# Kernel optimization log

Hardware: AMD Instinct MI355X
Metric: run time of the kernel (lower is better)

Reference implementation:

```python
import jax, jax.numpy as jnp
import numpy as np

PHI = 1.6
JITTER = 1e-4
ETA = 1.0
BETA = 0.5
EPS_CHOL = 1e-6
R_NEIGH = 2


def _solve3(L, d):
    # lower-triangular 3x3 forward substitution; L broadcasts against d[..., 3]
    y0 = d[..., 0] / L[..., 0, 0]
    y1 = (d[..., 1] - L[..., 1, 0] * y0) / L[..., 1, 1]
    y2 = (d[..., 2] - L[..., 2, 0] * y0 - L[..., 2, 1] * y1) / L[..., 2, 2]
    return jnp.stack([y0, y1, y2], axis=-1)


def _overlap_score(delta, L):
    # fused_gaussian_overlap_score: Gaussian log-overlap ~ -0.5*(Mahalanobis + logdet)
    y = _solve3(L, delta)
    maha = jnp.sum(y * y, axis=-1)
    logdet = 2.0 * jnp.sum(jnp.log(jnp.diagonal(L, axis1=-2, axis2=-1)), axis=-1)
    return -0.5 * (maha + logdet)


def _head(x, ln_g, ln_b, W1, b1, W2, b2):
    # LayerNorm -> Linear -> SiLU -> Linear(->1), squeeze
    m = jnp.mean(x, axis=-1, keepdims=True)
    v = jnp.var(x, axis=-1, keepdims=True)
    h = (x - m) / jnp.sqrt(v + 1e-5) * ln_g + ln_b
    h = jax.nn.silu(h @ W1 + b1)
    return (h @ W2 + b2)[..., 0]


def setup_inputs() -> dict:
    key = jax.random.key(0)
    ks = jax.random.split(key, 12)
    B, Kp, M, C = 2, 1024, 8, 256
    s_parent = jax.random.normal(ks[0], (B, Kp, C), jnp.float32)
    mu_p = jax.random.normal(ks[1], (B, Kp, 3), jnp.float32) * 10.0
    A = jax.random.normal(ks[2], (B, Kp, 3, 3), jnp.float32) * 0.5
    Sigma_p = jnp.einsum('bkij,bklj->bkil', A, A) + 0.05 * jnp.eye(3, dtype=jnp.float32)
    mask_parent = jnp.ones((B, Kp), jnp.float32)
    xi_noise = jax.random.normal(ks[3], (B, Kp, M, 3), jnp.float32)
    emb = jax.random.normal(ks[4], (M, C), jnp.float32) * 0.02
    lin = lambda k, fi, fo, s=0.02: jax.random.normal(k, (fi, fo), jnp.float32) * s
    return dict(
        s_parent=s_parent, mu_p=mu_p, Sigma_p=Sigma_p, mask_parent=mask_parent,
        xi_noise=xi_noise, emb=emb,
        gate_ln_g=jnp.ones((C,), jnp.float32), gate_ln_b=jnp.zeros((C,), jnp.float32),
        gate_W1=lin(ks[5], C, C), gate_b1=jnp.zeros((C,), jnp.float32),
        gate_W2=lin(ks[6], C, 1), gate_b2=jnp.zeros((1,), jnp.float32),
        prior_ln_g=jnp.ones((C,), jnp.float32), prior_ln_b=jnp.zeros((C,), jnp.float32),
        prior_W1=lin(ks[7], C, C), prior_b1=jnp.zeros((C,), jnp.float32),
        prior_W2=lin(ks[8], C, 1), prior_b2=jnp.zeros((1,), jnp.float32),
        geom_W=lin(ks[9], C, 3, 0.01), geom_b=jnp.zeros((3,), jnp.float32),
        K_target=6144,
    )


def reference(s_parent, mu_p, Sigma_p, mask_parent, xi_noise, emb,
              gate_ln_g, gate_ln_b, gate_W1, gate_b1, gate_W2, gate_b2,
              prior_ln_g, prior_ln_b, prior_W1, prior_b1, prior_W2, prior_b2,
              geom_W, geom_b, K_target):
    B, Kp, C = s_parent.shape
    M = emb.shape[0]
    Kc = Kp * M
    I3 = jnp.eye(3, dtype=s_parent.dtype)

    # --- candidate children from per-parent Cholesky splat ---
    Lp = jnp.linalg.cholesky(Sigma_p + EPS_CHOL * I3)               # [B,Kp,3,3]
    xi = xi_noise + (emb @ geom_W + geom_b)                          # [B,Kp,M,3]
    mu0 = mu_p[:, :, None, :] + jnp.einsum('bkae,bkme->bkma', Lp, xi)
    mu0 = mu0.reshape(B, Kc, 3)

    j0 = jnp.repeat(jnp.arange(Kp), M)                               # [Kc] birth parent
    t_ids = jnp.tile(jnp.arange(M), Kp)                              # [Kc] child slot
    m0 = mask_parent[:, j0]

    # --- gate g ---
    gate_in = s_parent[:, j0, :] + emb[t_ids]                        # [B,Kc,C]
    b = _head(gate_in, gate_ln_g, gate_ln_b, gate_W1, gate_b1, gate_W2, gate_b2)
    a = jax.nn.softplus(_head(s_parent, prior_ln_g, prior_ln_b, prior_W1, prior_b1, prior_W2, prior_b2))
    b = b + BETA * jnp.log(a[:, j0] + 1e-8)
    g = jax.nn.sigmoid(b / max(ETA, 1e-6)) * m0                      # [B,Kc]
    loss_count = jnp.mean((jnp.sum(g, axis=1) - float(K_target)) ** 2)

    # --- top-R neighbor parents by overlap score (indices only, no grad) ---
    mu0_birth = mu_p[:, j0, :]                                       # mu of birth parent
    delta1 = mu0_birth[:, :, None, :] - mu_p[:, None, :, :]          # [B,Kc,Kp,3]
    score1 = _overlap_score(delta1, Lp[:, None])                     # [B,Kc,Kp]
    self_hot = (jnp.arange(Kp)[None, :] == j0[:, None])              # [Kc,Kp]
    score1 = jnp.where(self_hot[None], 1e9, score1)
    _, neigh = jax.lax.top_k(jax.lax.stop_gradient(score1), R_NEIGH) # [B,Kc,R], col0=j0

    bidx = jnp.arange(B)[:, None, None]
    mu_nei = mu_p[bidx, neigh]                                       # [B,Kc,R,3]
    Sig_nei = Sigma_p[bidx, neigh]                                   # [B,Kc,R,3,3]
    L_nei = Lp[bidx, neigh]
    s_nei = s_parent[bidx, neigh]                                    # [B,Kc,R,C]

    # --- soft responsibilities over the R neighbors ---
    score2 = _overlap_score(mu0[:, :, None, :] - mu_nei, L_nei)      # [B,Kc,R]
    w = jax.nn.softmax(score2, axis=-1)

    # --- moment-matching refine (sparse form of B_resp: rows of B are w scattered at neigh) ---
    mu_child = jnp.einsum('bir,bird->bid', w, mu_nei)                # [B,Kc,3]
    intra = jnp.einsum('bir,birmn->bimn', w, Sig_nei) * PHI ** (-2)
    dmu = mu_nei - mu_child[:, :, None, :]
    inter = jnp.einsum('bir,birm,birn->bimn', w, dmu, dmu)
    Sigma_child = intra + inter + JITTER * I3                        # [B,Kc,3,3]

    s_mix = jnp.einsum('bir,birc->bic', w, s_nei)
    s_child0 = g[..., None] * s_mix                                  # [B,Kc,C]
    return s_child0, mu_child, Sigma_child, g, loss_count
```

## Files before the change

### kernel.cpp

```cpp
#include <hip/hip_runtime.h>
#include <math.h>

#define NPAR 2048
#define KP   1024
#define MM   8
#define CC   256
#define KC   8192
#define NCH  16384

#define WS_PKL    0
#define WS_PKI    8192
#define WS_PKM    16384
#define WS_L22    24576
#define WS_MEANSP 26624
#define WS_SUMSQ  28672
#define WS_DOT8   30720
#define WS_APRIOR 47104
#define WS_EGATE  49152
#define WS_UGATE  51200
#define WS_C0GATE 51456
#define WS_GEO    51712
#define WS_MEANE  51736
#define WS_SUMSQE 51744
#define WS_NEIGH  51752
#define WS_PGATE  53824

#define OUT_S    0
#define OUT_MU   4194304
#define OUT_SIG  4243456
#define OUT_G    4390912
#define OUT_LOSS 4407296

__device__ __forceinline__ float siluf(float x){ return x / (1.f + expf(-x)); }
__device__ __forceinline__ float softplusf(float x){ return x > 20.f ? x : log1pf(expf(x)); }

__global__ __launch_bounds__(256) void kP1(const float* __restrict__ sp,
                                           const float* __restrict__ mu_p,
                                           const float* __restrict__ Sig,
                                           const float* __restrict__ emb,
                                           const float* __restrict__ geom_W,
                                           const float* __restrict__ geom_b,
                                           float* __restrict__ ws) {
  int blk = blockIdx.x;
  int t = threadIdx.x;
  if (blk < 512) {
    int pid  = blk * 4 + (t >> 6);
    int lane = t & 63;
    const float4 v = *(const float4*)(sp + pid * CC + lane * 4);
    float s  = v.x + v.y + v.z + v.w;
    float ss = v.x*v.x + v.y*v.y + v.z*v.z + v.w*v.w;
    float pd[8];
#pragma unroll
    for (int m = 0; m < 8; m++) {
      float4 e = *(const float4*)(emb + m * CC + lane * 4);
      pd[m] = v.x*e.x + v.y*e.y + v.z*e.z + v.w*e.w;
    }
#pragma unroll
    for (int o = 32; o > 0; o >>= 1) {
      s  += __shfl_xor(s, o);
      ss += __shfl_xor(ss, o);
#pragma unroll
      for (int m = 0; m < 8; m++) pd[m] += __shfl_xor(pd[m], o);
    }
    if (lane == 0) {
      ws[WS_MEANSP + pid] = s * (1.f / 256.f);
      ws[WS_SUMSQ + pid]  = ss;
#pragma unroll
      for (int m = 0; m < 8; m++) ws[WS_DOT8 + pid * 8 + m] = pd[m];
    }
  } else if (blk < 520) {
    int pid = (blk - 512) * 256 + t;
    const float* S = Sig + pid * 9;
    float a00 = S[0] + 1e-6f, a10 = S[3], a11 = S[4] + 1e-6f;
    float a20 = S[6], a21 = S[7], a22 = S[8] + 1e-6f;
    float L00 = sqrtf(a00); float i0 = 1.f / L00;
    float L10 = a10 * i0, L20 = a20 * i0;
    float L11 = sqrtf(a11 - L10 * L10); float i1 = 1.f / L11;
    float L21 = (a21 - L20 * L10) * i1;
    float L22 = sqrtf(a22 - L20 * L20 - L21 * L21); float i2 = 1.f / L22;
    float logdet = 2.f * logf(L00 * L11 * L22);
    float4 pkl = {L10, L20, L21, logdet};
    float4 pki = {i0, i1, i2, L00};
    float4 pkm = {mu_p[pid*3+0], mu_p[pid*3+1], mu_p[pid*3+2], L11};
    *(float4*)(ws + WS_PKL + pid * 4) = pkl;
    *(float4*)(ws + WS_PKI + pid * 4) = pki;
    *(float4*)(ws + WS_PKM + pid * 4) = pkm;
    ws[WS_L22 + pid] = L22;
  } else {
    if (t < 192) {
      int o = t >> 3, lane8 = t & 7;
      int m = o / 3, d = o % 3;
      float acc = 0.f;
      for (int k = lane8; k < 256; k += 8) acc += emb[m * 256 + k] * geom_W[k * 3 + d];
      acc += __shfl_xor(acc, 1); acc += __shfl_xor(acc, 2); acc += __shfl_xor(acc, 4);
      if (lane8 == 0) ws[WS_GEO + o] = acc + geom_b[d];
    } else {
      int o = (t - 192) >> 3, lane8 = t & 7;
      if (o < 8) {
        float s = 0.f, ss = 0.f;
        for (int k = lane8; k < 256; k += 8) { float e = emb[o * 256 + k]; s += e; ss += e * e; }
        s  += __shfl_xor(s, 1);  s  += __shfl_xor(s, 2);  s  += __shfl_xor(s, 4);
        ss += __shfl_xor(ss, 1); ss += __shfl_xor(ss, 2); ss += __shfl_xor(ss, 4);
        if (lane8 == 0) { ws[WS_MEANE + o] = s * (1.f / 256.f); ws[WS_SUMSQE + o] = ss; }
      }
    }
  }
}

__global__ __launch_bounds__(256) void kP2(const float* __restrict__ sp,
                                           const float* __restrict__ emb,
                                           const float* __restrict__ g_ln_g,
                                           const float* __restrict__ g_ln_b,
                                           const float* __restrict__ gW1,
                                           const float* __restrict__ gb1,
                                           const float* __restrict__ p_ln_g,
                                           const float* __restrict__ p_ln_b,
                                           const float* __restrict__ pW1,
                                           const float* __restrict__ pb1,
                                           const float* __restrict__ pW2,
                                           const float* __restrict__ pb2,
                                           float* __restrict__ ws) {
  __shared__ float xs[8][256];
  __shared__ float red[4][8];
  __shared__ float redS[4][8];
  __shared__ float redQ[4][8];
  __shared__ float mv[2][8];
  int blk = blockIdx.x;
  int t = threadIdx.x;

  if (blk < 512) {
    int wv = blk * 4 + (t >> 6);
    int lane = t & 63;
    int b = wv >> 10;
    int j = wv & (KP - 1);
    const float4 qm = *(const float4*)(ws + WS_PKM + wv * 4);
    float qx = qm.x, qy = qm.y, qz = qm.z;
    float best = -3.4e38f; int bidx = 1 << 30;
    for (int it = 0; it < 16; it++) {
      int k = it * 64 + lane;
      int idx = b * KP + k;
      float4 pl = *(const float4*)(ws + WS_PKL + idx * 4);
      float4 pi = *(const float4*)(ws + WS_PKI + idx * 4);
      float4 pm = *(const float4*)(ws + WS_PKM + idx * 4);
      float dx = qx - pm.x, dy = qy - pm.y, dz = qz - pm.z;
      float y0 = dx * pi.x;
      float y1 = (dy - pl.x * y0) * pi.y;
      float y2 = (dz - pl.y * y0 - pl.z * y1) * pi.z;
      float sc = -0.5f * (y0*y0 + y1*y1 + y2*y2 + pl.w);
      if (k == j) sc = -3.4e38f;
      if (sc > best || (sc == best && k < bidx)) { best = sc; bidx = k; }
    }
#pragma unroll
    for (int o = 32; o > 0; o >>= 1) {
      float ob = __shfl_xor(best, o);
      int   oi = __shfl_xor(bidx, o);
      if (ob > best || (ob == best && oi < bidx)) { best = ob; bidx = oi; }
    }
    if (lane == 0) ((int*)ws)[WS_NEIGH + wv] = bidx;
  } else {
    int cblk = blk - 512;
    bool prior = (cblk >= 256 && cblk < 512);
    const float* W1 = prior ? pW1 : gW1;

    if (cblk < 256) {
      int base = cblk * 8;
      float g = g_ln_g[t];
#pragma unroll
      for (int r = 0; r < 8; r++) xs[r][t] = sp[(base + r) * 256 + t] * g;
    } else if (cblk < 512) {
      int base = (cblk - 256) * 8;
      float vr[8], s1[8], s2[8];
#pragma unroll
      for (int r = 0; r < 8; r++) {
        vr[r] = sp[(base + r) * 256 + t];
        s1[r] = vr[r];
        s2[r] = vr[r] * vr[r];
      }
#pragma unroll
      for (int o = 32; o > 0; o >>= 1) {
#pragma unroll
        for (int r = 0; r < 8; r++) { s1[r] += __shfl_xor(s1[r], o); s2[r] += __shfl_xor(s2[r], o); }
      }
      int wave = t >> 6;
      if ((t & 63) == 0) {
#pragma unroll
        for (int r = 0; r < 8; r++) { redS[wave][r] = s1[r]; redQ[wave][r] = s2[r]; }
      }
      __syncthreads();
      if (t < 8) {
        float sum = redS[0][t] + redS[1][t] + redS[2][t] + redS[3][t];
        float sq  = redQ[0][t] + redQ[1][t] + redQ[2][t] + redQ[3][t];
        float mean = sum * (1.f / 256.f);
        float var  = sq * (1.f / 256.f) - mean * mean;
        mv[0][t] = mean;
        mv[1][t] = rsqrtf(var + 1e-5f);
      }
      __syncthreads();
      float pg = p_ln_g[t], pbv = p_ln_b[t];
#pragma unroll
      for (int r = 0; r < 8; r++)
        xs[r][t] = (vr[r] - mv[0][r]) * mv[1][r] * pg + pbv;
    } else if (cblk == 512) {
      float g = g_ln_g[t];
#pragma unroll
      for (int r = 0; r < 8; r++) xs[r][t] = emb[r * 256 + t] * g;
    } else {
      xs[0][t] = g_ln_g[t];
      xs[1][t] = g_ln_b[t];
#pragma unroll
      for (int r = 2; r < 8; r++) xs[r][t] = 0.f;
    }
    __syncthreads();

    float acc[8] = {0,0,0,0,0,0,0,0};
    for (int k4 = 0; k4 < 256; k4 += 4) {
      float w0 = W1[(k4+0) * 256 + t];
      float w1 = W1[(k4+1) * 256 + t];
      float w2 = W1[(k4+2) * 256 + t];
      float w3 = W1[(k4+3) * 256 + t];
#pragma unroll
      for (int r = 0; r < 8; r++) {
        float4 x4 = *(const float4*)&xs[r][k4];
        acc[r] += x4.x * w0 + x4.y * w1 + x4.z * w2 + x4.w * w3;
      }
    }

    if (cblk < 256) {
      int base = cblk * 8;
#pragma unroll
      for (int r = 0; r < 8; r++) ws[WS_PGATE + (base + r) * 256 + t] = acc[r];
    } else if (cblk < 512) {
      int base = (cblk - 256) * 8;
      float b1 = pb1[t], w2 = pW2[t];
      float tv[8];
#pragma unroll
      for (int r = 0; r < 8; r++) {
        float h = acc[r] + b1;
        tv[r] = siluf(h) * w2;
      }
#pragma unroll
      for (int o = 32; o > 0; o >>= 1) {
#pragma unroll
        for (int r = 0; r < 8; r++) tv[r] += __shfl_xor(tv[r], o);
      }
      int wave = t >> 6;
      if ((t & 63) == 0) {
#pragma unroll
        for (int r = 0; r < 8; r++) red[wave][r] = tv[r];
      }
      __syncthreads();
      if (t < 8) {
        float sum = red[0][t] + red[1][t] + red[2][t] + red[3][t] + pb2[0];
        ws[WS_APRIOR + base + t] = softplusf(sum);
      }
    } else if (cblk == 512) {
#pragma unroll
      for (int r = 0; r < 8; r++) ws[WS_EGATE + r * 256 + t] = acc[r];
    } else {
      ws[WS_UGATE + t]  = acc[0];
      ws[WS_C0GATE + t] = acc[1] + gb1[t];
    }
  }
}

__global__ __launch_bounds__(256) void kD(const float* __restrict__ sp,
                                          const float* __restrict__ Sig,
                                          const float* __restrict__ mask,
                                          const float* __restrict__ xi_noise,
                                          const float* __restrict__ gW2,
                                          const float* __restrict__ gb2,
                                          const float* __restrict__ ws,
                                          float* __restrict__ out) {
  int wv   = blockIdx.x * 4 + (threadIdx.x >> 6);
  int lane = threadIdx.x & 63;
  int b = wv >> 13;
  int i = wv & (KC - 1);
  int j = i >> 3;
  int m = i & 7;
  int prow = b * KP + j;

  float mean_x = ws[WS_MEANSP + prow] + ws[WS_MEANE + m];
  float Ex2 = ws[WS_SUMSQ + prow] + 2.f * ws[WS_DOT8 + prow * 8 + m] + ws[WS_SUMSQE + m];
  float var = Ex2 * (1.f / 256.f) - mean_x * mean_x;
  float rstd = rsqrtf(var + 1e-5f);

  int c4 = lane * 4;
  float Pv[4], Ev[4], Uv[4], C0v[4], W2v[4];
  *(float4*)Pv  = *(const float4*)(ws + WS_PGATE + prow * 256 + c4);
  *(float4*)Ev  = *(const float4*)(ws + WS_EGATE + m * 256 + c4);
  *(float4*)Uv  = *(const float4*)(ws + WS_UGATE + c4);
  *(float4*)C0v = *(const float4*)(ws + WS_C0GATE + c4);
  *(float4*)W2v = *(const float4*)(gW2 + c4);
  float partial = 0.f;
#pragma unroll
  for (int q = 0; q < 4; q++) {
    float pre = (Pv[q] + Ev[q] - mean_x * Uv[q]) * rstd + C0v[q];
    partial += siluf(pre) * W2v[q];
  }
#pragma unroll
  for (int o = 32; o > 0; o >>= 1) partial += __shfl_xor(partial, o);
  float aP = ws[WS_APRIOR + prow];
  float bval = partial + gb2[0] + 0.5f * logf(aP + 1e-8f);
  float g = (1.f / (1.f + expf(-bval))) * mask[prow];

  const float4 plP = *(const float4*)(ws + WS_PKL + prow * 4);
  const float4 piP = *(const float4*)(ws + WS_PKI + prow * 4);
  const float4 pmP = *(const float4*)(ws + WS_PKM + prow * 4);
  float L22 = ws[WS_L22 + prow];

  int xbase = (prow * 8 + m) * 3;
  float x0 = xi_noise[xbase + 0] + ws[WS_GEO + m * 3 + 0];
  float x1 = xi_noise[xbase + 1] + ws[WS_GEO + m * 3 + 1];
  float x2 = xi_noise[xbase + 2] + ws[WS_GEO + m * 3 + 2];
  float m0x = pmP.x + piP.w * x0;
  float m0y = pmP.y + plP.x * x0 + pmP.w * x1;
  float m0z = pmP.z + plP.y * x0 + plP.z * x1 + L22 * x2;

  int n1 = ((const int*)ws)[WS_NEIGH + prow];
  int nrow1 = b * KP + n1;
  const float4 plN = *(const float4*)(ws + WS_PKL + nrow1 * 4);
  const float4 piN = *(const float4*)(ws + WS_PKI + nrow1 * 4);
  const float4 pmN = *(const float4*)(ws + WS_PKM + nrow1 * 4);

  float sc[2], nx[2], ny[2], nz[2];
  {
    float dx = m0x - pmP.x, dy = m0y - pmP.y, dz = m0z - pmP.z;
    float y0 = dx * piP.x;
    float y1 = (dy - plP.x * y0) * piP.y;
    float y2 = (dz - plP.y * y0 - plP.z * y1) * piP.z;
    sc[0] = -0.5f * (y0*y0 + y1*y1 + y2*y2 + plP.w);
    nx[0] = pmP.x; ny[0] = pmP.y; nz[0] = pmP.z;
  }
  {
    float dx = m0x - pmN.x, dy = m0y - pmN.y, dz = m0z - pmN.z;
    float y0 = dx * piN.x;
    float y1 = (dy - plN.x * y0) * piN.y;
    float y2 = (dz - plN.y * y0 - plN.z * y1) * piN.z;
    sc[1] = -0.5f * (y0*y0 + y1*y1 + y2*y2 + plN.w);
    nx[1] = pmN.x; ny[1] = pmN.y; nz[1] = pmN.z;
  }
  float mxs = fmaxf(sc[0], sc[1]);
  float e0 = expf(sc[0] - mxs), e1 = expf(sc[1] - mxs);
  float inv = 1.f / (e0 + e1);
  float w0 = e0 * inv, w1 = e1 * inv;

  float mcx = w0 * nx[0] + w1 * nx[1];
  float mcy = w0 * ny[0] + w1 * ny[1];
  float mcz = w0 * nz[0] + w1 * nz[1];

  float d0x = nx[0] - mcx, d0y = ny[0] - mcy, d0z = nz[0] - mcz;
  float d1x = nx[1] - mcx, d1y = ny[1] - mcy, d1z = nz[1] - mcz;
  const float* S0 = Sig + prow * 9;
  const float* S1 = Sig + nrow1 * 9;
  const float PHIm2 = 0.390625f;
  float Sout[9];
  float dd0[3] = {d0x, d0y, d0z};
  float dd1[3] = {d1x, d1y, d1z};
#pragma unroll
  for (int a = 0; a < 3; a++)
#pragma unroll
    for (int e = 0; e < 3; e++) {
      float v = (w0 * S0[a*3+e] + w1 * S1[a*3+e]) * PHIm2
              + w0 * dd0[a] * dd0[e] + w1 * dd1[a] * dd1[e];
      if (a == e) v += 1e-4f;
      Sout[a*3+e] = v;
    }

  if (lane == 0) {
    float* om = out + OUT_MU + wv * 3;
    om[0] = mcx; om[1] = mcy; om[2] = mcz;
    out[OUT_G + wv] = g;
    float* os = out + OUT_SIG + wv * 9;
#pragma unroll
    for (int q = 0; q < 9; q++) os[q] = Sout[q];
  }

  float s0v[4], s1v[4], ov[4];
  *(float4*)s0v = *(const float4*)(sp + prow * 256 + c4);
  *(float4*)s1v = *(const float4*)(sp + nrow1 * 256 + c4);
  float gw0 = g * w0, gw1 = g * w1;
#pragma unroll
  for (int q = 0; q < 4; q++) ov[q] = gw0 * s0v[q] + gw1 * s1v[q];
  *(float4*)(out + OUT_S + wv * 256 + c4) = *(float4*)ov;
}

__global__ __launch_bounds__(256) void kF(const float* __restrict__ out_in,
                                          const int* __restrict__ Kt,
                                          float* __restrict__ out) {
  __shared__ float red[4][2];
  int t = threadIdx.x;
  const float* gp = out_in + OUT_G;
  float s0 = 0.f, s1 = 0.f;
  for (int it = 0; it < 32; it++) {
    s0 += gp[it * 256 + t];
    s1 += gp[KC + it * 256 + t];
  }
#pragma unroll
  for (int o = 32; o > 0; o >>= 1) {
    s0 += __shfl_xor(s0, o);
    s1 += __shfl_xor(s1, o);
  }
  int wave = t >> 6;
  if ((t & 63) == 0) { red[wave][0] = s0; red[wave][1] = s1; }
  __syncthreads();
  if (t == 0) {
    float S0 = red[0][0] + red[1][0] + red[2][0] + red[3][0];
    float S1 = red[0][1] + red[1][1] + red[2][1] + red[3][1];
    float K = (float)Kt[0];
    float l0 = S0 - K, l1 = S1 - K;
    out[OUT_LOSS] = 0.5f * (l0 * l0 + l1 * l1);
  }
}

extern "C" void kernel_launch(void* const* d_in, const int* in_sizes, int n_in,
                              void* d_out, int out_size, void* d_ws, size_t ws_size,
                              hipStream_t stream) {
  const float* s_parent   = (const float*)d_in[0];
  const float* mu_p       = (const float*)d_in[1];
  const float* Sigma_p    = (const float*)d_in[2];
  const float* mask_par   = (const float*)d_in[3];
  const float* xi_noise   = (const float*)d_in[4];
  const float* emb        = (const float*)d_in[5];
  const float* gate_ln_g  = (const float*)d_in[6];
  const float* gate_ln_b  = (const float*)d_in[7];
  const float* gate_W1    = (const float*)d_in[8];
  const float* gate_b1    = (const float*)d_in[9];
  const float* gate_W2    = (const float*)d_in[10];
  const float* gate_b2    = (const float*)d_in[11];
  const float* prior_ln_g = (const float*)d_in[12];
  const float* prior_ln_b = (const float*)d_in[13];
  const float* prior_W1   = (const float*)d_in[14];
  const float* prior_b1   = (const float*)d_in[15];
  const float* prior_W2   = (const float*)d_in[16];
  const float* prior_b2   = (const float*)d_in[17];
  const float* geom_W     = (const float*)d_in[18];
  const float* geom_b     = (const float*)d_in[19];
  const int*   K_target   = (const int*)d_in[20];

  float* ws  = (float*)d_ws;
  float* out = (float*)d_out;

  kP1<<<521, 256, 0, stream>>>(s_parent, mu_p, Sigma_p, emb, geom_W, geom_b, ws);
  kP2<<<1026, 256, 0, stream>>>(s_parent, emb, gate_ln_g, gate_ln_b, gate_W1, gate_b1,
                                prior_ln_g, prior_ln_b, prior_W1, prior_b1,
                                prior_W2, prior_b2, ws);
  kD<<<NCH / 4, 256, 0, stream>>>(s_parent, Sigma_p, mask_par, xi_noise,
                                  gate_W2, gate_b2, ws, out);
  kF<<<1, 256, 0, stream>>>(out, K_target, out);
}
```

Baseline: 151.7 us.

## Merge preprocessing kernels, recompute Cholesky per block into LDS, pre-reduce gate sums

Folds the two preprocessing kernels into one launch. Each neighbor-search block recomputes the Cholesky factors and means for its whole batch into shared memory instead of reading them from a prior kernel. The per-parent stats (mean, sum of squares, embedding dot products) move into the gate-head blocks, and the geometry/embedding stats get their own extra block. kD now writes per-block gate partial sums so the final reduction reads 4096 values instead of 16384. This removes one launch and its dependency, at the cost of redundant Cholesky work per block and 40KB of LDS, which may lower occupancy.

```diff
diff --git a/kernel.cpp b/kernel.cpp
--- a/kernel.cpp
+++ b/kernel.cpp
@@ -24,6 +24,7 @@
 #define WS_SUMSQE 51744
 #define WS_NEIGH  51752
 #define WS_PGATE  53824
+#define WS_GPART  578112
 
 #define OUT_S    0
 #define OUT_MU   4194304
@@ -34,119 +35,79 @@
 __device__ __forceinline__ float siluf(float x){ return x / (1.f + expf(-x)); }
 __device__ __forceinline__ float softplusf(float x){ return x > 20.f ? x : log1pf(expf(x)); }
 
-__global__ __launch_bounds__(256) void kP1(const float* __restrict__ sp,
-                                           const float* __restrict__ mu_p,
-                                           const float* __restrict__ Sig,
-                                           const float* __restrict__ emb,
-                                           const float* __restrict__ geom_W,
-                                           const float* __restrict__ geom_b,
-                                           float* __restrict__ ws) {
+__global__ __launch_bounds__(256) void kA(const float* __restrict__ sp,
+                                          const float* __restrict__ mu_p,
+                                          const float* __restrict__ Sig,
+                                          const float* __restrict__ emb,
+                                          const float* __restrict__ geom_W,
+                                          const float* __restrict__ geom_b,
+                                          const float* __restrict__ g_ln_g,
+                                          const float* __restrict__ g_ln_b,
+                                          const float* __restrict__ gW1,
+                                          const float* __restrict__ gb1,
+                                          const float* __restrict__ p_ln_g,
+                                          const float* __restrict__ p_ln_b,
+                                          const float* __restrict__ pW1,
+                                          const float* __restrict__ pb1,
+                                          const float* __restrict__ pW2,
+                                          const float* __restrict__ pb2,
+                                          float* __restrict__ ws) {
+  __shared__ float smem[10 * 1024];
   int blk = blockIdx.x;
   int t = threadIdx.x;
+
   if (blk < 512) {
-    int pid  = blk * 4 + (t >> 6);
-    int lane = t & 63;
-    const float4 v = *(const float4*)(sp + pid * CC + lane * 4);
-    float s  = v.x + v.y + v.z + v.w;
-    float ss = v.x*v.x + v.y*v.y + v.z*v.z + v.w*v.w;
-    float pd[8];
-#pragma unroll
-    for (int m = 0; m < 8; m++) {
-      float4 e = *(const float4*)(emb + m * CC + lane * 4);
-      pd[m] = v.x*e.x + v.y*e.y + v.z*e.z + v.w*e.w;
-    }
-#pragma unroll
-    for (int o = 32; o > 0; o >>= 1) {
-      s  += __shfl_xor(s, o);
-      ss += __shfl_xor(ss, o);
-#pragma unroll
-      for (int m = 0; m < 8; m++) pd[m] += __shfl_xor(pd[m], o);
-    }
-    if (lane == 0) {
-      ws[WS_MEANSP + pid] = s * (1.f / 256.f);
-      ws[WS_SUMSQ + pid]  = ss;
-#pragma unroll
-      for (int m = 0; m < 8; m++) ws[WS_DOT8 + pid * 8 + m] = pd[m];
-    }
-  } else if (blk < 520) {
-    int pid = (blk - 512) * 256 + t;
-    const float* S = Sig + pid * 9;
-    float a00 = S[0] + 1e-6f, a10 = S[3], a11 = S[4] + 1e-6f;
-    float a20 = S[6], a21 = S[7], a22 = S[8] + 1e-6f;
-    float L00 = sqrtf(a00); float i0 = 1.f / L00;
-    float L10 = a10 * i0, L20 = a20 * i0;
-    float L11 = sqrtf(a11 - L10 * L10); float i1 = 1.f / L11;
-    float L21 = (a21 - L20 * L10) * i1;
-    float L22 = sqrtf(a22 - L20 * L20 - L21 * L21); float i2 = 1.f / L22;
-    float logdet = 2.f * logf(L00 * L11 * L22);
-    float4 pkl = {L10, L20, L21, logdet};
-    float4 pki = {i0, i1, i2, L00};
-    float4 pkm = {mu_p[pid*3+0], mu_p[pid*3+1], mu_p[pid*3+2], L11};
-    *(float4*)(ws + WS_PKL + pid * 4) = pkl;
-    *(float4*)(ws + WS_PKI + pid * 4) = pki;
-    *(float4*)(ws + WS_PKM + pid * 4) = pkm;
-    ws[WS_L22 + pid] = L22;
-  } else {
-    if (t < 192) {
-      int o = t >> 3, lane8 = t & 7;
-      int m = o / 3, d = o % 3;
-      float acc = 0.f;
-      for (int k = lane8; k < 256; k += 8) acc += emb[m * 256 + k] * geom_W[k * 3 + d];
-      acc += __shfl_xor(acc, 1); acc += __shfl_xor(acc, 2); acc += __shfl_xor(acc, 4);
-      if (lane8 == 0) ws[WS_GEO + o] = acc + geom_b[d];
-    } else {
-      int o = (t - 192) >> 3, lane8 = t & 7;
-      if (o < 8) {
-        float s = 0.f, ss = 0.f;
-        for (int k = lane8; k < 256; k += 8) { float e = emb[o * 256 + k]; s += e; ss += e * e; }
-        s  += __shfl_xor(s, 1);  s  += __shfl_xor(s, 2);  s  += __shfl_xor(s, 4);
-        ss += __shfl_xor(ss, 1); ss += __shfl_xor(ss, 2); ss += __shfl_xor(ss, 4);
-        if (lane8 == 0) { ws[WS_MEANE + o] = s * (1.f / 256.f); ws[WS_SUMSQE + o] = ss; }
-      }
-    }
-  }
-}
-
-__global__ __launch_bounds__(256) void kP2(const float* __restrict__ sp,
-                                           const float* __restrict__ emb,
-                                           const float* __restrict__ g_ln_g,
-                                           const float* __restrict__ g_ln_b,
-                                           const float* __restrict__ gW1,
-                                           const float* __restrict__ gb1,
-                                           const float* __restrict__ p_ln_g,
-                                           const float* __restrict__ p_ln_b,
-                                           const float* __restrict__ pW1,
-                                           const float* __restrict__ pb1,
-                                           const float* __restrict__ pW2,
-                                           const float* __restrict__ pb2,
-                                           float* __restrict__ ws) {
-  __shared__ float xs[8][256];
-  __shared__ float red[4][8];
-  __shared__ float redS[4][8];
-  __shared__ float redQ[4][8];
-  __shared__ float mv[2][8];
-  int blk = blockIdx.x;
-  int t = threadIdx.x;
-
-  if (blk < 512) {
+    int b = blk >> 8;
+#pragma unroll
+    for (int q = 0; q < 4; q++) {
+      int loc = q * 256 + t;
+      int pid = b * KP + loc;
+      const float* S = Sig + pid * 9;
+      float a00 = S[0] + 1e-6f, a10 = S[3], a11 = S[4] + 1e-6f;
+      float a20 = S[6], a21 = S[7], a22 = S[8] + 1e-6f;
+      float L00 = sqrtf(a00); float i0 = 1.f / L00;
+      float L10 = a10 * i0, L20 = a20 * i0;
+      float L11 = sqrtf(a11 - L10 * L10); float i1 = 1.f / L11;
+      float L21 = (a21 - L20 * L10) * i1;
+      float L22 = sqrtf(a22 - L20 * L20 - L21 * L21); float i2 = 1.f / L22;
+      float logdet = 2.f * logf(L00 * L11 * L22);
+      float mx = mu_p[pid * 3 + 0], my = mu_p[pid * 3 + 1], mz = mu_p[pid * 3 + 2];
+      smem[0 * 1024 + loc] = L10;
+      smem[1 * 1024 + loc] = L20;
+      smem[2 * 1024 + loc] = L21;
+      smem[3 * 1024 + loc] = logdet;
+      smem[4 * 1024 + loc] = i0;
+      smem[5 * 1024 + loc] = i1;
+      smem[6 * 1024 + loc] = i2;
+      smem[7 * 1024 + loc] = mx;
+      smem[8 * 1024 + loc] = my;
+      smem[9 * 1024 + loc] = mz;
+      if ((loc >> 2) == (blk & 255)) {
+        float4 pkl = {L10, L20, L21, logdet};
+        float4 pki = {i0, i1, i2, L00};
+        float4 pkm = {mx, my, mz, L11};
+        *(float4*)(ws + WS_PKL + pid * 4) = pkl;
+        *(float4*)(ws + WS_PKI + pid * 4) = pki;
+        *(float4*)(ws + WS_PKM + pid * 4) = pkm;
+        ws[WS_L22 + pid] = L22;
+      }
+    }
+    __syncthreads();
+
     int wv = blk * 4 + (t >> 6);
     int lane = t & 63;
-    int b = wv >> 10;
     int j = wv & (KP - 1);
-    const float4 qm = *(const float4*)(ws + WS_PKM + wv * 4);
-    float qx = qm.x, qy = qm.y, qz = qm.z;
+    float qx = smem[7 * 1024 + j], qy = smem[8 * 1024 + j], qz = smem[9 * 1024 + j];
     float best = -3.4e38f; int bidx = 1 << 30;
     for (int it = 0; it < 16; it++) {
       int k = it * 64 + lane;
-      int idx = b * KP + k;
-      float4 pl = *(const float4*)(ws + WS_PKL + idx * 4);
-      float4 pi = *(const float4*)(ws + WS_PKI + idx * 4);
-      float4 pm = *(const float4*)(ws + WS_PKM + idx * 4);
-      float dx = qx - pm.x, dy = qy - pm.y, dz = qz - pm.z;
-      float y0 = dx * pi.x;
-      float y1 = (dy - pl.x * y0) * pi.y;
-      float y2 = (dz - pl.y * y0 - pl.z * y1) * pi.z;
-      float sc = -0.5f * (y0*y0 + y1*y1 + y2*y2 + pl.w);
+      float dx = qx - smem[7 * 1024 + k];
+      float dy = qy - smem[8 * 1024 + k];
+      float dz = qz - smem[9 * 1024 + k];
+      float y0 = dx * smem[4 * 1024 + k];
+      float y1 = (dy - smem[0 * 1024 + k] * y0) * smem[5 * 1024 + k];
+      float y2 = (dz - smem[1 * 1024 + k] * y0 - smem[2 * 1024 + k] * y1) * smem[6 * 1024 + k];
+      float sc = -0.5f * (y0 * y0 + y1 * y1 + y2 * y2 + smem[3 * 1024 + k]);
       if (k == j) sc = -3.4e38f;
       if (sc > best || (sc == best && k < bidx)) { best = sc; bidx = k; }
     }
@@ -158,6 +119,13 @@
     }
     if (lane == 0) ((int*)ws)[WS_NEIGH + wv] = bidx;
   } else {
+    float (*xs)[256] = (float(*)[256])smem;
+    float* statred   = smem + 2048;
+    float (*redS)[8] = (float(*)[8])(smem + 2432);
+    float (*redQ)[8] = (float(*)[8])(smem + 2464);
+    float (*mv)[8]   = (float(*)[8])(smem + 2496);
+    float (*red)[8]  = (float(*)[8])(smem + 2528);
+
     int cblk = blk - 512;
     bool prior = (cblk >= 256 && cblk < 512);
     const float* W1 = prior ? pW1 : gW1;
@@ -165,8 +133,50 @@
     if (cblk < 256) {
       int base = cblk * 8;
       float g = g_ln_g[t];
-#pragma unroll
-      for (int r = 0; r < 8; r++) xs[r][t] = sp[(base + r) * 256 + t] * g;
+      float vr[8], em[8];
+#pragma unroll
+      for (int r = 0; r < 8; r++) vr[r] = sp[(base + r) * 256 + t];
+#pragma unroll
+      for (int m = 0; m < 8; m++) em[m] = emb[m * 256 + t];
+#pragma unroll
+      for (int r = 0; r < 8; r++) xs[r][t] = vr[r] * g;
+      int wave = t >> 6, lane = t & 63;
+#pragma unroll
+      for (int r = 0; r < 8; r++) {
+        float p0 = vr[r], p1 = vr[r] * vr[r];
+        float d[8];
+#pragma unroll
+        for (int m = 0; m < 8; m++) d[m] = vr[r] * em[m];
+#pragma unroll
+        for (int o = 32; o > 0; o >>= 1) {
+          p0 += __shfl_xor(p0, o);
+          p1 += __shfl_xor(p1, o);
+#pragma unroll
+          for (int m = 0; m < 8; m++) d[m] += __shfl_xor(d[m], o);
+        }
+        if (lane == 0) {
+          float* dst = statred + (wave * 8 + r) * 10;
+          dst[0] = p0; dst[1] = p1;
+#pragma unroll
+          for (int m = 0; m < 8; m++) dst[2 + m] = d[m];
+        }
+      }
+      __syncthreads();
+      if (t < 8) {
+        int r = t;
+        float s = 0.f, ss = 0.f, dd[8] = {0, 0, 0, 0, 0, 0, 0, 0};
+#pragma unroll
+        for (int w = 0; w < 4; w++) {
+          float* srcp = statred + (w * 8 + r) * 10;
+          s += srcp[0]; ss += srcp[1];
+#pragma unroll
+          for (int m = 0; m < 8; m++) dd[m] += srcp[2 + m];
+        }
+        ws[WS_MEANSP + base + r] = s * (1.f / 256.f);
+        ws[WS_SUMSQ + base + r]  = ss;
+#pragma unroll
+        for (int m = 0; m < 8; m++) ws[WS_DOT8 + (base + r) * 8 + m] = dd[m];
+      }
     } else if (cblk < 512) {
       int base = (cblk - 256) * 8;
       float vr[8], s1[8], s2[8];
@@ -204,20 +214,39 @@
       float g = g_ln_g[t];
 #pragma unroll
       for (int r = 0; r < 8; r++) xs[r][t] = emb[r * 256 + t] * g;
-    } else {
+    } else if (cblk == 513) {
       xs[0][t] = g_ln_g[t];
       xs[1][t] = g_ln_b[t];
 #pragma unroll
       for (int r = 2; r < 8; r++) xs[r][t] = 0.f;
+    } else {
+      if (t < 192) {
+        int o = t >> 3, lane8 = t & 7;
+        int m = o / 3, d = o % 3;
+        float acc = 0.f;
+        for (int k = lane8; k < 256; k += 8) acc += emb[m * 256 + k] * geom_W[k * 3 + d];
+        acc += __shfl_xor(acc, 1); acc += __shfl_xor(acc, 2); acc += __shfl_xor(acc, 4);
+        if (lane8 == 0) ws[WS_GEO + o] = acc + geom_b[d];
+      } else {
+        int o = (t - 192) >> 3, lane8 = t & 7;
+        if (o < 8) {
+          float s = 0.f, ss = 0.f;
+          for (int k = lane8; k < 256; k += 8) { float e = emb[o * 256 + k]; s += e; ss += e * e; }
+          s  += __shfl_xor(s, 1);  s  += __shfl_xor(s, 2);  s  += __shfl_xor(s, 4);
+          ss += __shfl_xor(ss, 1); ss += __shfl_xor(ss, 2); ss += __shfl_xor(ss, 4);
+          if (lane8 == 0) { ws[WS_MEANE + o] = s * (1.f / 256.f); ws[WS_SUMSQE + o] = ss; }
+        }
+      }
+      return;
     }
     __syncthreads();
 
-    float acc[8] = {0,0,0,0,0,0,0,0};
+    float acc[8] = {0, 0, 0, 0, 0, 0, 0, 0};
     for (int k4 = 0; k4 < 256; k4 += 4) {
-      float w0 = W1[(k4+0) * 256 + t];
-      float w1 = W1[(k4+1) * 256 + t];
-      float w2 = W1[(k4+2) * 256 + t];
-      float w3 = W1[(k4+3) * 256 + t];
+      float w0 = W1[(k4 + 0) * 256 + t];
+      float w1 = W1[(k4 + 1) * 256 + t];
+      float w2 = W1[(k4 + 2) * 256 + t];
+      float w3 = W1[(k4 + 3) * 256 + t];
 #pragma unroll
       for (int r = 0; r < 8; r++) {
         float4 x4 = *(const float4*)&xs[r][k4];
@@ -269,8 +298,9 @@
                                           const float* __restrict__ xi_noise,
                                           const float* __restrict__ gW2,
                                           const float* __restrict__ gb2,
-                                          const float* __restrict__ ws,
+                                          float* __restrict__ ws,
                                           float* __restrict__ out) {
+  __shared__ float gpart[4];
   int wv   = blockIdx.x * 4 + (threadIdx.x >> 6);
   int lane = threadIdx.x & 63;
   int b = wv >> 13;
@@ -303,6 +333,11 @@
   float bval = partial + gb2[0] + 0.5f * logf(aP + 1e-8f);
   float g = (1.f / (1.f + expf(-bval))) * mask[prow];
 
+  if (lane == 0) gpart[threadIdx.x >> 6] = g;
+  __syncthreads();
+  if (threadIdx.x == 0)
+    ws[WS_GPART + blockIdx.x] = gpart[0] + gpart[1] + gpart[2] + gpart[3];
+
   const float4 plP = *(const float4*)(ws + WS_PKL + prow * 4);
   const float4 piP = *(const float4*)(ws + WS_PKI + prow * 4);
   const float4 pmP = *(const float4*)(ws + WS_PKM + prow * 4);
@@ -384,16 +419,17 @@
   *(float4*)(out + OUT_S + wv * 256 + c4) = *(float4*)ov;
 }
 
-__global__ __launch_bounds__(256) void kF(const float* __restrict__ out_in,
+__global__ __launch_bounds__(256) void kF(const float* __restrict__ ws,
                                           const int* __restrict__ Kt,
                                           float* __restrict__ out) {
   __shared__ float red[4][2];
   int t = threadIdx.x;
-  const float* gp = out_in + OUT_G;
+  const float* gp = ws + WS_GPART;
   float s0 = 0.f, s1 = 0.f;
-  for (int it = 0; it < 32; it++) {
+#pragma unroll
+  for (int it = 0; it < 8; it++) {
     s0 += gp[it * 256 + t];
-    s1 += gp[KC + it * 256 + t];
+    s1 += gp[2048 + it * 256 + t];
   }
 #pragma unroll
   for (int o = 32; o > 0; o >>= 1) {
@@ -440,11 +476,11 @@
   float* ws  = (float*)d_ws;
   float* out = (float*)d_out;
 
-  kP1<<<521, 256, 0, stream>>>(s_parent, mu_p, Sigma_p, emb, geom_W, geom_b, ws);
-  kP2<<<1026, 256, 0, stream>>>(s_parent, emb, gate_ln_g, gate_ln_b, gate_W1, gate_b1,
-                                prior_ln_g, prior_ln_b, prior_W1, prior_b1,
-                                prior_W2, prior_b2, ws);
+  kA<<<1027, 256, 0, stream>>>(s_parent, mu_p, Sigma_p, emb, geom_W, geom_b,
+                               gate_ln_g, gate_ln_b, gate_W1, gate_b1,
+                               prior_ln_g, prior_ln_b, prior_W1, prior_b1,
+                               prior_W2, prior_b2, ws);
   kD<<<NCH / 4, 256, 0, stream>>>(s_parent, Sigma_p, mask_par, xi_noise,
                                   gate_W2, gate_b2, ws, out);
-  kF<<<1, 256, 0, stream>>>(out, K_target, out);
+  kF<<<1, 256, 0, stream>>>(ws, K_target, out);
 }
```

After: 146.1 us. 1.04x faster.
